# Optimization experiments

Measured on AMD Instinct MI355X. Metric: run time of the kernel, lower is better.

Reference implementation:

```python
import jax, jax.numpy as jnp
import numpy as np

H = 32  # hid_dim (hard-coded in the module)


def _lstm_dir(xs, h0, c0, Wih, Whh, b):
    # xs: [S, B, Din]; PyTorch gate order i, f, g, o
    def step(carry, xt):
        h, c = carry
        g = xt @ Wih.T + h @ Whh.T + b
        i, f, gg, o = jnp.split(g, 4, axis=-1)
        c = jax.nn.sigmoid(f) * c + jax.nn.sigmoid(i) * jnp.tanh(gg)
        h = jax.nn.sigmoid(o) * jnp.tanh(c)
        return (h, c), h
    (hT, cT), ys = jax.lax.scan(step, (h0, c0), xs)
    return ys, hT, cT


def _bilstm(xs, h0s, c0s, Wih, Whh, b):
    yf, hf, cf = _lstm_dir(xs, h0s[0], c0s[0], Wih[0], Whh[0], b[0])
    yb, hb, cb = _lstm_dir(xs[::-1], h0s[1], c0s[1], Wih[1], Whh[1], b[1])
    return jnp.concatenate([yf, yb[::-1]], -1), jnp.stack([hf, hb]), jnp.stack([cf, cb])


def _forward(rain_hist, feature, h0, c0, W_mlp, b_mlp, Wih_g, Whh_g, b_ih_g, b_hh_g,
             Wih0, Whh0, b0, Wih1, Whh1, b1, W_fc, b_fc):
    B, hist_len, C, _ = rain_hist.shape

    def step(carry, feat_t):
        xn, hn, cn = carry  # xn [B,C,1], hn/cn [4,B,H]
        x = jnp.concatenate([xn, feat_t], -1)                 # [B,C,in_dim]
        g = jax.nn.sigmoid(x.reshape(B, -1) @ W_mlp + b_mlp)  # gated graph MLP
        x = jnp.concatenate([g.reshape(B, C, 1), x], -1)      # [B,C,in_dim+1]
        # GRU cell on city-pooled input, updating all 4 layer-dir hidden slices
        u = x.mean(axis=1)                                    # [B,in_dim+1]
        gx = u @ Wih_g + b_ih_g                               # [B,3H]
        gh = hn @ Whh_g + b_hh_g                              # [4,B,3H]
        rx, zx, nx = jnp.split(gx, 3, -1)
        rh, zh, nh = jnp.split(gh, 3, -1)
        r = jax.nn.sigmoid(rx + rh)
        z = jax.nn.sigmoid(zx + zh)
        n = jnp.tanh(nx + r * nh)
        hn = (1.0 - z) * n + z * hn
        # 2-layer bidirectional LSTM over the city axis
        xs = x.transpose(1, 0, 2)                             # [C,B,in_dim+1]
        y0, h0n, c0n = _bilstm(xs, hn[0:2], cn[0:2], Wih0, Whh0, b0)
        y1, h1n, c1n = _bilstm(y0, hn[2:4], cn[2:4], Wih1, Whh1, b1)
        hn = jnp.concatenate([h0n, h1n], 0)
        cn = jnp.concatenate([c0n, c1n], 0)
        xn = y1[..., :H].transpose(1, 0, 2) @ W_fc + b_fc     # [B,C,1]
        return (xn, hn, cn), xn

    feats = feature[:, hist_len:].transpose(1, 0, 2, 3)       # [pred_len,B,C,in_dim-1]
    _, preds = jax.lax.scan(step, (rain_hist[:, -1], h0, c0), feats)
    return preds.transpose(1, 0, 2, 3)                        # [B,pred_len,C,1]


def setup_inputs():
    key = jax.random.key(0)
    ks = jax.random.split(key, 18)
    B, hist_len, pred_len, C, in_dim = 512, 24, 24, 184, 14
    D = in_dim + 1
    s = 0.1
    r = lambda i, shape: (jax.random.normal(ks[i], shape, jnp.float32) * s)
    return {
        "rain_hist": jax.random.normal(ks[0], (B, hist_len, C, 1), jnp.float32),
        "feature": jax.random.normal(ks[1], (B, hist_len + pred_len, C, in_dim - 1), jnp.float32),
        "h0": jax.random.normal(ks[2], (4, B, H), jnp.float32),
        "c0": jax.random.normal(ks[3], (4, B, H), jnp.float32),
        "W_mlp": r(4, (C * in_dim, C)),
        "b_mlp": r(5, (C,)),
        "Wih_g": r(6, (D, 3 * H)),
        "Whh_g": r(7, (H, 3 * H)),
        "b_ih_g": r(8, (3 * H,)),
        "b_hh_g": r(9, (3 * H,)),
        "Wih0": r(10, (2, 4 * H, D)),
        "Whh0": r(11, (2, 4 * H, H)),
        "b0": r(12, (2, 4 * H)),
        "Wih1": r(13, (2, 4 * H, 2 * H)),
        "Whh1": r(14, (2, 4 * H, H)),
        "b1": r(15, (2, 4 * H)),
        "W_fc": r(16, (H, 1)),
        "b_fc": r(17, (1,)),
    }


def reference(rain_hist, feature, h0, c0, W_mlp, b_mlp, Wih_g, Whh_g, b_ih_g, b_hh_g,
              Wih0, Whh0, b0, Wih1, Whh1, b1, W_fc, b_fc):
    return _forward(rain_hist, feature, h0, c0, W_mlp, b_mlp, Wih_g, Whh_g, b_ih_g, b_hh_g,
                    Wih0, Whh0, b0, Wih1, Whh1, b1, W_fc, b_fc)
```

## Files before the change

### kernel.cpp

```cpp
#include <hip/hip_runtime.h>

#define CC   184
#define HLEN 24
#define PLEN 24
#define IND  14
#define DD   15
#define HB   32
#define BB   512

__device__ __forceinline__ float sigm(float x)  { return 1.0f / (1.0f + __expf(-x)); }
__device__ __forceinline__ float tanhx(float x) { return 1.0f - 2.0f / (1.0f + __expf(2.0f * x)); }

__global__ __launch_bounds__(256, 2) void bilstm_kernel(
    const float* __restrict__ rain_hist,
    const float* __restrict__ feature,
    const float* __restrict__ h0,
    const float* __restrict__ c0,
    const float* __restrict__ W_mlp,
    const float* __restrict__ b_mlp,
    const float* __restrict__ Wih_g,
    const float* __restrict__ Whh_g,
    const float* __restrict__ b_ih_g,
    const float* __restrict__ b_hh_g,
    const float* __restrict__ Wih0,
    const float* __restrict__ Whh0,
    const float* __restrict__ b0,
    const float* __restrict__ Wih1,
    const float* __restrict__ Whh1,
    const float* __restrict__ b1,
    const float* __restrict__ W_fc,
    const float* __restrict__ b_fc,
    float* __restrict__ out)
{
    const int b   = blockIdx.x;
    const int tid = threadIdx.x;

    __shared__ float xs[CC][16];
    __shared__ float y0buf[CC][2*HB];
    __shared__ float hn[4][HB];
    __shared__ float cn[4][HB];
    __shared__ float hcur[2][HB];
    __shared__ float gates[2][4*HB];
    __shared__ float gxbuf[3*HB];
    __shared__ float ghbuf[4][3*HB];
    __shared__ float ubuf[DD];
    __shared__ float xn_lds[CC];

    const int d  = tid >> 7;
    const int gi = tid & 127;
    const int dd = tid >> 5;
    const int kk = tid & 31;

    for (int idx = tid; idx < 4 * HB; idx += 256) {
        int l = idx >> 5, k = idx & 31;
        hn[l][k] = h0[(l * BB + b) * HB + k];
        cn[l][k] = c0[(l * BB + b) * HB + k];
    }
    for (int c = tid; c < CC; c += 256)
        xs[c][1] = rain_hist[(b * HLEN + (HLEN - 1)) * CC + c];
    __syncthreads();

    float creg = 0.0f;
    float wreg[64];
    float whreg[HB];
    float breg = 0.0f;

    #pragma unroll 1
    for (int t = 0; t < PLEN; ++t) {
        const float* ft = feature + ((size_t)b * (HLEN + PLEN) + (HLEN + t)) * CC * 13;
        for (int idx = tid; idx < CC * 13; idx += 256) {
            int c = idx / 13, f = idx - c * 13;
            xs[c][2 + f] = ft[idx];
        }
        __syncthreads();

        if (tid < CC) {
            float a0 = b_mlp[tid], a1 = 0.f, a2 = 0.f, a3 = 0.f;
            const float* w = W_mlp + tid;
            #pragma unroll 1
            for (int c = 0; c < CC; ++c) {
                #pragma unroll
                for (int f = 0; f < IND; ++f) {
                    float p = xs[c][1 + f] * w[f * CC];
                    if ((f & 3) == 0)      a0 += p;
                    else if ((f & 3) == 1) a1 += p;
                    else if ((f & 3) == 2) a2 += p;
                    else                   a3 += p;
                }
                w += IND * CC;
            }
            xs[tid][0] = sigm(a0 + a1 + a2 + a3);
        }
        __syncthreads();

        if (tid < DD) {
            float a0 = 0.f, a1 = 0.f, a2 = 0.f, a3 = 0.f;
            for (int c = 0; c < CC; c += 4) {
                a0 += xs[c][tid]; a1 += xs[c + 1][tid];
                a2 += xs[c + 2][tid]; a3 += xs[c + 3][tid];
            }
            ubuf[tid] = (a0 + a1 + a2 + a3) * (1.0f / CC);
        }
        __syncthreads();

        if (tid < 96) {
            float a = b_ih_g[tid];
            #pragma unroll
            for (int k = 0; k < DD; ++k) a += ubuf[k] * Wih_g[k * 96 + tid];
            gxbuf[tid] = a;
        }
        for (int idx = tid; idx < 4 * 96; idx += 256) {
            int l = idx / 96, j = idx - l * 96;
            float a = b_hh_g[j];
            #pragma unroll
            for (int k = 0; k < HB; ++k) a += hn[l][k] * Whh_g[k * 96 + j];
            ghbuf[l][j] = a;
        }
        __syncthreads();
        if (tid < 128) {
            int l = tid >> 5, k = tid & 31;
            float r = sigm(gxbuf[k] + ghbuf[l][k]);
            float z = sigm(gxbuf[HB + k] + ghbuf[l][HB + k]);
            float n = tanhx(gxbuf[2 * HB + k] + r * ghbuf[l][2 * HB + k]);
            hn[l][k] = (1.0f - z) * n + z * hn[l][k];
        }
        __syncthreads();

        {
            const int row = d * 128 + gi;
            #pragma unroll
            for (int k = 0; k < DD; ++k) wreg[k] = Wih0[row * DD + k];
            #pragma unroll
            for (int k = 0; k < HB; ++k) whreg[k] = Whh0[row * HB + k];
            breg = b0[row];
        }
        if (tid < 64) {
            hcur[dd][kk] = hn[dd][kk];
            creg = cn[dd][kk];
        }
        __syncthreads();

        #pragma unroll 1
        for (int ci = 0; ci < CC; ++ci) {
            const int xc = d ? (CC - 1 - ci) : ci;
            float a0 = breg, a1 = 0.f, a2 = 0.f, a3 = 0.f;
            #pragma unroll
            for (int k = 0; k < DD; ++k) {
                float p = xs[xc][k] * wreg[k];
                if ((k & 3) == 0)      a0 += p;
                else if ((k & 3) == 1) a1 += p;
                else if ((k & 3) == 2) a2 += p;
                else                   a3 += p;
            }
            #pragma unroll
            for (int k = 0; k < HB; ++k) {
                float p = hcur[d][k] * whreg[k];
                if ((k & 3) == 0)      a0 += p;
                else if ((k & 3) == 1) a1 += p;
                else if ((k & 3) == 2) a2 += p;
                else                   a3 += p;
            }
            gates[d][gi] = a0 + a1 + a2 + a3;
            __syncthreads();
            if (tid < 64) {
                const int xc2 = dd ? (CC - 1 - ci) : ci;
                float iv = sigm(gates[dd][kk]);
                float fv = sigm(gates[dd][HB + kk]);
                float gv = tanhx(gates[dd][2 * HB + kk]);
                float ov = sigm(gates[dd][3 * HB + kk]);
                creg = fv * creg + iv * gv;
                float hv = ov * tanhx(creg);
                hcur[dd][kk] = hv;
                y0buf[xc2][dd * HB + kk] = hv;
            }
            __syncthreads();
        }
        if (tid < 64) {
            hn[dd][kk] = hcur[dd][kk];
            cn[dd][kk] = creg;
        }
        __syncthreads();

        {
            const int row = d * 128 + gi;
            #pragma unroll
            for (int k = 0; k < 2 * HB; ++k) wreg[k] = Wih1[row * 2 * HB + k];
            #pragma unroll
            for (int k = 0; k < HB; ++k) whreg[k] = Whh1[row * HB + k];
            breg = b1[row];
        }
        if (tid < 64) {
            hcur[dd][kk] = hn[2 + dd][kk];
            creg = cn[2 + dd][kk];
        }
        __syncthreads();

        const float wfc = (tid < 64) ? W_fc[kk] : 0.f;
        const float bfc = b_fc[0];

        #pragma unroll 1
        for (int ci = 0; ci < CC; ++ci) {
            const int xc = d ? (CC - 1 - ci) : ci;
            float a0 = breg, a1 = 0.f, a2 = 0.f, a3 = 0.f;
            #pragma unroll
            for (int k = 0; k < 2 * HB; ++k) {
                float p = y0buf[xc][k] * wreg[k];
                if ((k & 3) == 0)      a0 += p;
                else if ((k & 3) == 1) a1 += p;
                else if ((k & 3) == 2) a2 += p;
                else                   a3 += p;
            }
            #pragma unroll
            for (int k = 0; k < HB; ++k) {
                float p = hcur[d][k] * whreg[k];
                if ((k & 3) == 0)      a0 += p;
                else if ((k & 3) == 1) a1 += p;
                else if ((k & 3) == 2) a2 += p;
                else                   a3 += p;
            }
            gates[d][gi] = a0 + a1 + a2 + a3;
            __syncthreads();
            if (tid < 64) {
                float iv = sigm(gates[dd][kk]);
                float fv = sigm(gates[dd][HB + kk]);
                float gv = tanhx(gates[dd][2 * HB + kk]);
                float ov = sigm(gates[dd][3 * HB + kk]);
                creg = fv * creg + iv * gv;
                float hv = ov * tanhx(creg);
                hcur[dd][kk] = hv;
                float contrib = hv * wfc;
                contrib += __shfl_xor(contrib, 16);
                contrib += __shfl_xor(contrib, 8);
                contrib += __shfl_xor(contrib, 4);
                contrib += __shfl_xor(contrib, 2);
                contrib += __shfl_xor(contrib, 1);
                if (tid == 0) {
                    float xnv = contrib + bfc;
                    xn_lds[ci] = xnv;
                    out[((size_t)b * PLEN + t) * CC + ci] = xnv;
                }
            }
            __syncthreads();
        }
        if (tid < 64) {
            hn[2 + dd][kk] = hcur[dd][kk];
            cn[2 + dd][kk] = creg;
        }
        __syncthreads();
        for (int c = tid; c < CC; c += 256) xs[c][1] = xn_lds[c];
        __syncthreads();
    }
}

extern "C" void kernel_launch(void* const* d_in, const int* in_sizes, int n_in,
                              void* d_out, int out_size, void* d_ws, size_t ws_size,
                              hipStream_t stream) {
    const float* rain_hist = (const float*)d_in[0];
    const float* feature   = (const float*)d_in[1];
    const float* h0        = (const float*)d_in[2];
    const float* c0        = (const float*)d_in[3];
    const float* W_mlp     = (const float*)d_in[4];
    const float* b_mlp     = (const float*)d_in[5];
    const float* Wih_g     = (const float*)d_in[6];
    const float* Whh_g     = (const float*)d_in[7];
    const float* b_ih_g    = (const float*)d_in[8];
    const float* b_hh_g    = (const float*)d_in[9];
    const float* Wih0      = (const float*)d_in[10];
    const float* Whh0      = (const float*)d_in[11];
    const float* b0        = (const float*)d_in[12];
    const float* Wih1      = (const float*)d_in[13];
    const float* Whh1      = (const float*)d_in[14];
    const float* b1        = (const float*)d_in[15];
    const float* W_fc      = (const float*)d_in[16];
    const float* b_fc      = (const float*)d_in[17];
    float* out = (float*)d_out;

    bilstm_kernel<<<dim3(BB), dim3(256), 0, stream>>>(
        rain_hist, feature, h0, c0, W_mlp, b_mlp, Wih_g, Whh_g, b_ih_g, b_hh_g,
        Wih0, Whh0, b0, Wih1, Whh1, b1, W_fc, b_fc, out);
}
```

Before: 7.719 ms.

## Fuse LSTM gate computation via wave shuffles, one barrier per step

The bidirectional LSTM steps are reorganised. Each wave now computes four gate rows for 16 hidden units and exchanges them with lane shuffles, so the separate gates buffer and its second barrier per recurrence step are gone. The input projection for the next city is computed after the barrier, overlapping with the recurrent dependency, and the hidden state is double-buffered. The output FC projection moves out of the serial loop into a parallel pass over an fp16 buffer of layer-1 forward outputs, which adds a small precision risk.

```diff
diff --git a/kernel.cpp b/kernel.cpp
--- a/kernel.cpp
+++ b/kernel.cpp
@@ -1,9 +1,10 @@
 #include <hip/hip_runtime.h>
+#include <hip/hip_fp16.h>
 
 #define CC   184
 #define HLEN 24
 #define PLEN 24
-#define IND  14
+#define SEQ  48
 #define DD   15
 #define HB   32
 #define BB   512
@@ -35,39 +36,46 @@
     const int b   = blockIdx.x;
     const int tid = threadIdx.x;
 
-    __shared__ float xs[CC][16];
-    __shared__ float y0buf[CC][2*HB];
-    __shared__ float hn[4][HB];
-    __shared__ float cn[4][HB];
-    __shared__ float hcur[2][HB];
-    __shared__ float gates[2][4*HB];
-    __shared__ float gxbuf[3*HB];
-    __shared__ float ghbuf[4][3*HB];
-    __shared__ float ubuf[DD];
-    __shared__ float xn_lds[CC];
-
-    const int d  = tid >> 7;
-    const int gi = tid & 127;
-    const int dd = tid >> 5;
-    const int kk = tid & 31;
+    __shared__ __align__(16) float xs[CC][16];
+    __shared__ __align__(16) float y0[CC][64];
+    __shared__ __half               y1f[HB][CC];
+    __shared__ __align__(16) float hn_l[4][HB];
+    __shared__ __align__(16) float cn_l[4][HB];
+    __shared__ __align__(16) float hbuf[2][2][HB];
+    __shared__ float gx[96];
+    __shared__ float gh[4][96];
+    __shared__ float ub[16];
+
+    const int l    = tid & 63;
+    const int w    = tid >> 6;
+    const int dir  = w >> 1;
+    const int sub  = w & 1;
+    const int g    = l >> 4;
+    const int kloc = l & 15;
+    const int k    = sub * 16 + kloc;
+    const int gb0  = (l >> 4) & 1;
+    const int gb1  = (l >> 5) & 1;
+    const int row  = g * 32 + k;
 
     for (int idx = tid; idx < 4 * HB; idx += 256) {
-        int l = idx >> 5, k = idx & 31;
-        hn[l][k] = h0[(l * BB + b) * HB + k];
-        cn[l][k] = c0[(l * BB + b) * HB + k];
+        int lx = idx >> 5, kx = idx & 31;
+        hn_l[lx][kx] = h0[(lx * BB + b) * HB + kx];
+        cn_l[lx][kx] = c0[(lx * BB + b) * HB + kx];
     }
-    for (int c = tid; c < CC; c += 256)
-        xs[c][1] = rain_hist[(b * HLEN + (HLEN - 1)) * CC + c];
+    for (int c = tid; c < CC; c += 256) {
+        xs[c][0]  = 0.0f;
+        xs[c][1]  = rain_hist[(b * HLEN + (HLEN - 1)) * CC + c];
+        xs[c][15] = 0.0f;
+    }
     __syncthreads();
 
-    float creg = 0.0f;
     float wreg[64];
     float whreg[HB];
-    float breg = 0.0f;
+    float breg;
 
     #pragma unroll 1
     for (int t = 0; t < PLEN; ++t) {
-        const float* ft = feature + ((size_t)b * (HLEN + PLEN) + (HLEN + t)) * CC * 13;
+        const float* ft = feature + ((size_t)b * SEQ + (HLEN + t)) * CC * 13;
         for (int idx = tid; idx < CC * 13; idx += 256) {
             int c = idx / 13, f = idx - c * 13;
             xs[c][2 + f] = ft[idx];
@@ -76,178 +84,203 @@
 
         if (tid < CC) {
             float a0 = b_mlp[tid], a1 = 0.f, a2 = 0.f, a3 = 0.f;
-            const float* w = W_mlp + tid;
+            const float* wp = W_mlp + tid;
             #pragma unroll 1
             for (int c = 0; c < CC; ++c) {
-                #pragma unroll
-                for (int f = 0; f < IND; ++f) {
-                    float p = xs[c][1 + f] * w[f * CC];
-                    if ((f & 3) == 0)      a0 += p;
-                    else if ((f & 3) == 1) a1 += p;
-                    else if ((f & 3) == 2) a2 += p;
-                    else                   a3 += p;
-                }
-                w += IND * CC;
-            }
-            xs[tid][0] = sigm(a0 + a1 + a2 + a3);
+                const float4* xq = (const float4*)&xs[c][0];
+                float4 q0 = xq[0], q1 = xq[1], q2 = xq[2], q3 = xq[3];
+                const float* wc = wp + c * 14 * 184;
+                a0 += wc[0 * 184] * q0.y;  a1 += wc[1 * 184] * q0.z;
+                a2 += wc[2 * 184] * q0.w;  a3 += wc[3 * 184] * q1.x;
+                a0 += wc[4 * 184] * q1.y;  a1 += wc[5 * 184] * q1.z;
+                a2 += wc[6 * 184] * q1.w;  a3 += wc[7 * 184] * q2.x;
+                a0 += wc[8 * 184] * q2.y;  a1 += wc[9 * 184] * q2.z;
+                a2 += wc[10 * 184] * q2.w; a3 += wc[11 * 184] * q3.x;
+                a0 += wc[12 * 184] * q3.y; a1 += wc[13 * 184] * q3.z;
+            }
+            xs[tid][0] = sigm((a0 + a1) + (a2 + a3));
         }
         __syncthreads();
 
         if (tid < DD) {
-            float a0 = 0.f, a1 = 0.f, a2 = 0.f, a3 = 0.f;
-            for (int c = 0; c < CC; c += 4) {
-                a0 += xs[c][tid]; a1 += xs[c + 1][tid];
-                a2 += xs[c + 2][tid]; a3 += xs[c + 3][tid];
-            }
-            ubuf[tid] = (a0 + a1 + a2 + a3) * (1.0f / CC);
+            float a = 0.f;
+            #pragma unroll 4
+            for (int c = 0; c < CC; ++c) a += xs[c][tid];
+            ub[tid] = a * (1.0f / CC);
         }
         __syncthreads();
 
         if (tid < 96) {
             float a = b_ih_g[tid];
             #pragma unroll
-            for (int k = 0; k < DD; ++k) a += ubuf[k] * Wih_g[k * 96 + tid];
-            gxbuf[tid] = a;
+            for (int m = 0; m < DD; ++m) a += ub[m] * Wih_g[m * 96 + tid];
+            gx[tid] = a;
         }
         for (int idx = tid; idx < 4 * 96; idx += 256) {
-            int l = idx / 96, j = idx - l * 96;
+            int lx = idx / 96, j = idx - lx * 96;
             float a = b_hh_g[j];
             #pragma unroll
-            for (int k = 0; k < HB; ++k) a += hn[l][k] * Whh_g[k * 96 + j];
-            ghbuf[l][j] = a;
+            for (int m = 0; m < HB; ++m) a += hn_l[lx][m] * Whh_g[m * 96 + j];
+            gh[lx][j] = a;
         }
         __syncthreads();
         if (tid < 128) {
-            int l = tid >> 5, k = tid & 31;
-            float r = sigm(gxbuf[k] + ghbuf[l][k]);
-            float z = sigm(gxbuf[HB + k] + ghbuf[l][HB + k]);
-            float n = tanhx(gxbuf[2 * HB + k] + r * ghbuf[l][2 * HB + k]);
-            hn[l][k] = (1.0f - z) * n + z * hn[l][k];
+            int lx = tid >> 5, kx = tid & 31;
+            float r = sigm(gx[kx] + gh[lx][kx]);
+            float z = sigm(gx[HB + kx] + gh[lx][HB + kx]);
+            float n = tanhx(gx[2 * HB + kx] + r * gh[lx][2 * HB + kx]);
+            hn_l[lx][kx] = (1.0f - z) * n + z * hn_l[lx][kx];
         }
         __syncthreads();
 
         {
-            const int row = d * 128 + gi;
-            #pragma unroll
-            for (int k = 0; k < DD; ++k) wreg[k] = Wih0[row * DD + k];
-            #pragma unroll
-            for (int k = 0; k < HB; ++k) whreg[k] = Whh0[row * HB + k];
-            breg = b0[row];
-        }
-        if (tid < 64) {
-            hcur[dd][kk] = hn[dd][kk];
-            creg = cn[dd][kk];
-        }
-        __syncthreads();
-
-        #pragma unroll 1
-        for (int ci = 0; ci < CC; ++ci) {
-            const int xc = d ? (CC - 1 - ci) : ci;
-            float a0 = breg, a1 = 0.f, a2 = 0.f, a3 = 0.f;
-            #pragma unroll
-            for (int k = 0; k < DD; ++k) {
-                float p = xs[xc][k] * wreg[k];
-                if ((k & 3) == 0)      a0 += p;
-                else if ((k & 3) == 1) a1 += p;
-                else if ((k & 3) == 2) a2 += p;
-                else                   a3 += p;
-            }
-            #pragma unroll
-            for (int k = 0; k < HB; ++k) {
-                float p = hcur[d][k] * whreg[k];
-                if ((k & 3) == 0)      a0 += p;
-                else if ((k & 3) == 1) a1 += p;
-                else if ((k & 3) == 2) a2 += p;
-                else                   a3 += p;
-            }
-            gates[d][gi] = a0 + a1 + a2 + a3;
-            __syncthreads();
-            if (tid < 64) {
-                const int xc2 = dd ? (CC - 1 - ci) : ci;
-                float iv = sigm(gates[dd][kk]);
-                float fv = sigm(gates[dd][HB + kk]);
-                float gv = tanhx(gates[dd][2 * HB + kk]);
-                float ov = sigm(gates[dd][3 * HB + kk]);
-                creg = fv * creg + iv * gv;
-                float hv = ov * tanhx(creg);
-                hcur[dd][kk] = hv;
-                y0buf[xc2][dd * HB + kk] = hv;
-            }
-            __syncthreads();
-        }
-        if (tid < 64) {
-            hn[dd][kk] = hcur[dd][kk];
-            cn[dd][kk] = creg;
+            const float* Wp = Wih0 + (dir * 128 + row) * DD;
+            #pragma unroll
+            for (int j = 0; j < DD; ++j) wreg[j] = Wp[j];
+            wreg[15] = 0.0f;
+            const float* Hp = Whh0 + (dir * 128 + row) * HB;
+            #pragma unroll
+            for (int m = 0; m < HB; ++m) whreg[m] = Hp[m];
+            breg = b0[dir * 128 + row];
+
+            float c_st = cn_l[dir][k];
+            float hv = 0.0f;
+
+            float xacc;
+            {
+                const int xc0 = dir ? (CC - 1) : 0;
+                const float4* xq = (const float4*)&xs[xc0][0];
+                float a0 = 0.f, a1 = 0.f, a2 = 0.f, a3 = 0.f;
+                #pragma unroll
+                for (int q = 0; q < 4; ++q) {
+                    float4 v = xq[q];
+                    a0 += v.x * wreg[4 * q];     a1 += v.y * wreg[4 * q + 1];
+                    a2 += v.z * wreg[4 * q + 2]; a3 += v.w * wreg[4 * q + 3];
+                }
+                xacc = (a0 + a1) + (a2 + a3);
+            }
+
+            #pragma unroll 1
+            for (int ci = 0; ci < CC; ++ci) {
+                const float* hsrc = (ci == 0) ? &hn_l[dir][0] : &hbuf[ci & 1][dir][0];
+                float a0 = xacc + breg, a1 = 0.f, a2 = 0.f, a3 = 0.f;
+                const float4* hq = (const float4*)hsrc;
+                #pragma unroll
+                for (int q = 0; q < 8; ++q) {
+                    float4 v = hq[q];
+                    a0 += v.x * whreg[4 * q];     a1 += v.y * whreg[4 * q + 1];
+                    a2 += v.z * whreg[4 * q + 2]; a3 += v.w * whreg[4 * q + 3];
+                }
+                float av  = (a0 + a1) + (a2 + a3);
+                float s16 = __shfl_xor(av, 16);
+                float s32 = __shfl_xor(av, 32);
+                float s48 = __shfl_xor(s16, 32);
+                float A0 = gb0 ? s16 : av,  A1 = gb0 ? av  : s16;
+                float B0 = gb0 ? s48 : s32, B1 = gb0 ? s32 : s48;
+                float iv = gb1 ? B0 : A0, fv = gb1 ? B1 : A1;
+                float gv = gb1 ? A0 : B0, ov = gb1 ? A1 : B1;
+                c_st = sigm(fv) * c_st + sigm(iv) * tanhx(gv);
+                hv   = sigm(ov) * tanhx(c_st);
+                const int xc = dir ? (CC - 1 - ci) : ci;
+                if (g == 0) {
+                    hbuf[(ci + 1) & 1][dir][k] = hv;
+                    y0[xc][dir * 32 + k] = hv;
+                }
+                __syncthreads();
+                if (ci + 1 < CC) {
+                    const int xcn = dir ? (CC - 2 - ci) : (ci + 1);
+                    const float4* xq = (const float4*)&xs[xcn][0];
+                    float b0_ = 0.f, b1_ = 0.f, b2_ = 0.f, b3_ = 0.f;
+                    #pragma unroll
+                    for (int q = 0; q < 4; ++q) {
+                        float4 v = xq[q];
+                        b0_ += v.x * wreg[4 * q];     b1_ += v.y * wreg[4 * q + 1];
+                        b2_ += v.z * wreg[4 * q + 2]; b3_ += v.w * wreg[4 * q + 3];
+                    }
+                    xacc = (b0_ + b1_) + (b2_ + b3_);
+                }
+            }
+            if (g == 0) { hn_l[dir][k] = hv; cn_l[dir][k] = c_st; }
         }
         __syncthreads();
 
         {
-            const int row = d * 128 + gi;
-            #pragma unroll
-            for (int k = 0; k < 2 * HB; ++k) wreg[k] = Wih1[row * 2 * HB + k];
-            #pragma unroll
-            for (int k = 0; k < HB; ++k) whreg[k] = Whh1[row * HB + k];
-            breg = b1[row];
-        }
-        if (tid < 64) {
-            hcur[dd][kk] = hn[2 + dd][kk];
-            creg = cn[2 + dd][kk];
-        }
-        __syncthreads();
-
-        const float wfc = (tid < 64) ? W_fc[kk] : 0.f;
-        const float bfc = b_fc[0];
-
-        #pragma unroll 1
-        for (int ci = 0; ci < CC; ++ci) {
-            const int xc = d ? (CC - 1 - ci) : ci;
-            float a0 = breg, a1 = 0.f, a2 = 0.f, a3 = 0.f;
-            #pragma unroll
-            for (int k = 0; k < 2 * HB; ++k) {
-                float p = y0buf[xc][k] * wreg[k];
-                if ((k & 3) == 0)      a0 += p;
-                else if ((k & 3) == 1) a1 += p;
-                else if ((k & 3) == 2) a2 += p;
-                else                   a3 += p;
-            }
-            #pragma unroll
-            for (int k = 0; k < HB; ++k) {
-                float p = hcur[d][k] * whreg[k];
-                if ((k & 3) == 0)      a0 += p;
-                else if ((k & 3) == 1) a1 += p;
-                else if ((k & 3) == 2) a2 += p;
-                else                   a3 += p;
-            }
-            gates[d][gi] = a0 + a1 + a2 + a3;
-            __syncthreads();
-            if (tid < 64) {
-                float iv = sigm(gates[dd][kk]);
-                float fv = sigm(gates[dd][HB + kk]);
-                float gv = tanhx(gates[dd][2 * HB + kk]);
-                float ov = sigm(gates[dd][3 * HB + kk]);
-                creg = fv * creg + iv * gv;
-                float hv = ov * tanhx(creg);
-                hcur[dd][kk] = hv;
-                float contrib = hv * wfc;
-                contrib += __shfl_xor(contrib, 16);
-                contrib += __shfl_xor(contrib, 8);
-                contrib += __shfl_xor(contrib, 4);
-                contrib += __shfl_xor(contrib, 2);
-                contrib += __shfl_xor(contrib, 1);
-                if (tid == 0) {
-                    float xnv = contrib + bfc;
-                    xn_lds[ci] = xnv;
-                    out[((size_t)b * PLEN + t) * CC + ci] = xnv;
-                }
-            }
-            __syncthreads();
-        }
-        if (tid < 64) {
-            hn[2 + dd][kk] = hcur[dd][kk];
-            cn[2 + dd][kk] = creg;
-        }
-        __syncthreads();
-        for (int c = tid; c < CC; c += 256) xs[c][1] = xn_lds[c];
+            const float* Wp = Wih1 + (dir * 128 + row) * 64;
+            #pragma unroll
+            for (int j = 0; j < 64; ++j) wreg[j] = Wp[j];
+            const float* Hp = Whh1 + (dir * 128 + row) * HB;
+            #pragma unroll
+            for (int m = 0; m < HB; ++m) whreg[m] = Hp[m];
+            breg = b1[dir * 128 + row];
+
+            float c_st = cn_l[2 + dir][k];
+            float hv = 0.0f;
+
+            float xacc;
+            {
+                const int xc0 = dir ? (CC - 1) : 0;
+                const float4* xq = (const float4*)&y0[xc0][0];
+                float a0 = 0.f, a1 = 0.f, a2 = 0.f, a3 = 0.f;
+                #pragma unroll
+                for (int q = 0; q < 16; ++q) {
+                    float4 v = xq[q];
+                    a0 += v.x * wreg[4 * q];     a1 += v.y * wreg[4 * q + 1];
+                    a2 += v.z * wreg[4 * q + 2]; a3 += v.w * wreg[4 * q + 3];
+                }
+                xacc = (a0 + a1) + (a2 + a3);
+            }
+
+            #pragma unroll 1
+            for (int ci = 0; ci < CC; ++ci) {
+                const float* hsrc = (ci == 0) ? &hn_l[2 + dir][0] : &hbuf[ci & 1][dir][0];
+                float a0 = xacc + breg, a1 = 0.f, a2 = 0.f, a3 = 0.f;
+                const float4* hq = (const float4*)hsrc;
+                #pragma unroll
+                for (int q = 0; q < 8; ++q) {
+                    float4 v = hq[q];
+                    a0 += v.x * whreg[4 * q];     a1 += v.y * whreg[4 * q + 1];
+                    a2 += v.z * whreg[4 * q + 2]; a3 += v.w * whreg[4 * q + 3];
+                }
+                float av  = (a0 + a1) + (a2 + a3);
+                float s16 = __shfl_xor(av, 16);
+                float s32 = __shfl_xor(av, 32);
+                float s48 = __shfl_xor(s16, 32);
+                float A0 = gb0 ? s16 : av,  A1 = gb0 ? av  : s16;
+                float B0 = gb0 ? s48 : s32, B1 = gb0 ? s32 : s48;
+                float iv = gb1 ? B0 : A0, fv = gb1 ? B1 : A1;
+                float gv = gb1 ? A0 : B0, ov = gb1 ? A1 : B1;
+                c_st = sigm(fv) * c_st + sigm(iv) * tanhx(gv);
+                hv   = sigm(ov) * tanhx(c_st);
+                if (g == 0) {
+                    hbuf[(ci + 1) & 1][dir][k] = hv;
+                    if (dir == 0) y1f[k][ci] = __float2half(hv);
+                }
+                __syncthreads();
+                if (ci + 1 < CC) {
+                    const int xcn = dir ? (CC - 2 - ci) : (ci + 1);
+                    const float4* xq = (const float4*)&y0[xcn][0];
+                    float b0_ = 0.f, b1_ = 0.f, b2_ = 0.f, b3_ = 0.f;
+                    #pragma unroll
+                    for (int q = 0; q < 16; ++q) {
+                        float4 v = xq[q];
+                        b0_ += v.x * wreg[4 * q];     b1_ += v.y * wreg[4 * q + 1];
+                        b2_ += v.z * wreg[4 * q + 2]; b3_ += v.w * wreg[4 * q + 3];
+                    }
+                    xacc = (b0_ + b1_) + (b2_ + b3_);
+                }
+            }
+            if (g == 0) { hn_l[2 + dir][k] = hv; cn_l[2 + dir][k] = c_st; }
+        }
+        __syncthreads();
+
+        if (tid < CC) {
+            float acc = b_fc[0];
+            #pragma unroll
+            for (int m = 0; m < HB; ++m)
+                acc += __half2float(y1f[m][tid]) * W_fc[m];
+            out[((size_t)b * PLEN + t) * CC + tid] = acc;
+            xs[tid][1] = acc;
+        }
         __syncthreads();
     }
 }
```

Result: slower. 10.64 ms (+37.8%).
